# Kernel tuning notes

Measured on AMD Instinct MI355X. Metric: run time of the kernel, lower is better.

The kernel has to match this reference:

```python
import jax, jax.numpy as jnp
import numpy as np

ID, IH, IW = 8, 16, 16
HEADS, DIM_HEAD = 8, 32
INP, OUP = 256, 256
B = 4
N = ID * IH * IW  # 2048
INNER = HEADS * DIM_HEAD  # 256
SCALE = DIM_HEAD ** -0.5


def _make_relative_pos():
    # Faithful to the torch ctor: 3D coords, pairwise diffs, linearize, shift to >=0
    z, y, x = np.meshgrid(np.arange(ID), np.arange(IH), np.arange(IW), indexing='ij')
    coords = np.stack([z.ravel(), y.ravel(), x.ravel()], axis=1)  # [N,3]
    rel = coords[:, None, :] - coords[None, :, :]                 # [N,N,3]
    rp = rel[:, :, 0] * (IH * IW) + rel[:, :, 1] * IW + rel[:, :, 2]
    rp = rp - rp.min()
    return jnp.asarray(rp, dtype=jnp.int32)                       # [N,N]


def setup_inputs() -> dict:
    key = jax.random.key(0)
    k1, k2, k3, k4, k5 = jax.random.split(key, 5)
    table_size = ID * IH * IW * 8  # 16384, as in nn.Embedding ctor
    return {
        "x": jax.random.normal(k1, (B, N, INP), dtype=jnp.float32),
        "w_qkv": jax.random.normal(k2, (INP, 3 * INNER), dtype=jnp.float32) * (INP ** -0.5),
        "bias_table": jax.random.normal(k3, (table_size, 1), dtype=jnp.float32),
        "w_out": jax.random.normal(k4, (INNER, OUP), dtype=jnp.float32) * (INNER ** -0.5),
        "b_out": jax.random.normal(k5, (OUP,), dtype=jnp.float32),
        "relative_pos": _make_relative_pos(),
    }


def reference(x, w_qkv, bias_table, w_out, b_out, relative_pos):
    Bb, Nn, C = x.shape
    qkv = x @ w_qkv                                   # [B, N, 3*H*D]
    qkv = qkv.reshape(Bb, Nn, 3, HEADS, DIM_HEAD)
    qkv = jnp.transpose(qkv, (2, 0, 3, 1, 4))         # [3, B, H, N, D]
    q, k, v = qkv[0], qkv[1], qkv[2]
    q = q * SCALE
    attn = jnp.einsum('bhnd,bhmd->bhnm', q, k)        # [B, H, N, N]
    bias = bias_table[relative_pos, 0]                # [N, N], shared across B,H
    attn = attn + bias
    attn = jax.nn.softmax(attn, axis=-1)
    out = jnp.einsum('bhnm,bhmd->bhnd', attn, v)      # [B, H, N, D]
    out = jnp.transpose(out, (0, 2, 1, 3)).reshape(Bb, Nn, INNER)
    return out @ w_out + b_out                        # dropout p=0 -> identity
```

## Files before the change

kernel.cpp:

```cpp
#include <hip/hip_runtime.h>

typedef unsigned short u16;
typedef unsigned int u32;
typedef __attribute__((ext_vector_type(8))) short bf16x8;
typedef __attribute__((ext_vector_type(4))) short bf16x4;
typedef __attribute__((ext_vector_type(4))) float f32x4;

#define MFMA16(a, b, c) __builtin_amdgcn_mfma_f32_16x16x32_bf16(a, b, c, 0, 0, 0)
#define MFMAK16(a, b, c) __builtin_amdgcn_mfma_f32_16x16x16bf16_1k(a, b, c, 0, 0, 0)

__device__ __forceinline__ float hw_exp2(float x) { return __builtin_amdgcn_exp2f(x); }

__device__ __forceinline__ u16 f2bf(float f) {
    union { float f; u32 i; } v; v.f = f;
    u32 x = v.i;
    return (u16)((x + 0x7FFFu + ((x >> 16) & 1u)) >> 16);
}

__global__ __launch_bounds__(256) void k_prep(const float* __restrict__ x,
                                              const float* __restrict__ wqkv,
                                              const float* __restrict__ wout,
                                              u16* __restrict__ xb,
                                              u16* __restrict__ wqkvT,
                                              u16* __restrict__ woutT) {
    const float QSCALE2 = 0.2550566756538019f;
    int bx = blockIdx.x, tid = threadIdx.x;
    if (bx < 1024) {
        int base = bx * 2048 + tid * 8;
        float4 a = *(const float4*)(x + base);
        float4 b = *(const float4*)(x + base + 4);
        uint4 r;
        r.x = f2bf(a.x) | ((u32)f2bf(a.y) << 16);
        r.y = f2bf(a.z) | ((u32)f2bf(a.w) << 16);
        r.z = f2bf(b.x) | ((u32)f2bf(b.y) << 16);
        r.w = f2bf(b.z) | ((u32)f2bf(b.w) << 16);
        *(uint4*)(xb + base) = r;
    } else if (bx < 1792) {
        int idx = (bx - 1024) * 256 + tid;
        int n = idx >> 8, kk = idx & 255;
        float sc = (n < 256) ? QSCALE2 : 1.0f;
        wqkvT[idx] = f2bf(wqkv[kk * 768 + n] * sc);
    } else {
        int idx = (bx - 1792) * 256 + tid;
        int n = idx >> 8, kk = idx & 255;
        woutT[idx] = f2bf(wout[kk * 256 + n]);
    }
}

__global__ __launch_bounds__(256) void k_gemm_qkv(const u16* __restrict__ xb,
                                                  const u16* __restrict__ wT,
                                                  u16* __restrict__ qkv) {
    __shared__ __align__(16) u16 slds[8704];
    const int tid = threadIdx.x;
    const int wave = tid >> 6, lane = tid & 63, quad = lane >> 4, ql = lane & 15;
    const int mbase = blockIdx.x * 128 + (wave & 1) * 64;
    const int nbase = blockIdx.y * 64 + (wave >> 1) * 32;
    f32x4 acc[4][2];
#pragma unroll
    for (int i = 0; i < 4; ++i)
#pragma unroll
        for (int j = 0; j < 2; ++j) acc[i][j] = (f32x4){0.f, 0.f, 0.f, 0.f};
#pragma unroll
    for (int ks = 0; ks < 8; ++ks) {
        bf16x8 af[4], bfm[2];
#pragma unroll
        for (int ms = 0; ms < 4; ++ms)
            af[ms] = *(const bf16x8*)(xb + (size_t)(mbase + ms * 16 + ql) * 256 + ks * 32 + quad * 8);
#pragma unroll
        for (int ns = 0; ns < 2; ++ns)
            bfm[ns] = *(const bf16x8*)(wT + (size_t)(nbase + ns * 16 + ql) * 256 + ks * 32 + quad * 8);
#pragma unroll
        for (int ms = 0; ms < 4; ++ms)
#pragma unroll
            for (int ns = 0; ns < 2; ++ns)
                acc[ms][ns] = MFMA16(af[ms], bfm[ns], acc[ms][ns]);
    }

    const int t = (blockIdx.y * 64) >> 8;
    if (t < 2) {
        const int rowb = (wave & 1) * 64, colb = (wave >> 1) * 32;
#pragma unroll
        for (int ms = 0; ms < 4; ++ms)
#pragma unroll
            for (int ns = 0; ns < 2; ++ns)
#pragma unroll
                for (int r = 0; r < 4; ++r)
                    slds[(rowb + ms * 16 + quad * 4 + r) * 68 + colb + ns * 16 + ql] =
                        f2bf(acc[ms][ns][r]);
        __syncthreads();
        u16* base = qkv + (size_t)t * 2097152;
#pragma unroll
        for (int p = 0; p < 8; ++p) {
            int c = p * 256 + tid;
            int row = c >> 4, ch = c & 15;
            uint2 w = *(const uint2*)&slds[row * 68 + ch * 4];
            int n = blockIdx.x * 128 + row;
            int col = blockIdx.y * 64 + ch * 4;
            int h = (col & 255) >> 5, d = col & 31;
            *(uint2*)(base + ((size_t)((n >> 11) * 8 + h) * 2048 + (n & 2047)) * 32 + d) = w;
        }
    } else {
        const int hl = wave >> 1, nb = (wave & 1) * 64;
#pragma unroll
        for (int ms = 0; ms < 4; ++ms)
#pragma unroll
            for (int ns = 0; ns < 2; ++ns) {
                u16 e0 = f2bf(acc[ms][ns][0]), e1 = f2bf(acc[ms][ns][1]);
                u16 e2 = f2bf(acc[ms][ns][2]), e3 = f2bf(acc[ms][ns][3]);
                uint2 pp; pp.x = e0 | ((u32)e1 << 16); pp.y = e2 | ((u32)e3 << 16);
                *(uint2*)&slds[(hl * 32 + ns * 16 + ql) * 136 + nb + ms * 16 + quad * 4] = pp;
            }
        __syncthreads();
        u16* vbase = qkv + (size_t)2 * 2097152;
#pragma unroll
        for (int p = 0; p < 4; ++p) {
            int c = p * 256 + tid;
            int row = c >> 4, ch = c & 15;
            bf16x8 w = *(const bf16x8*)&slds[row * 136 + ch * 8];
            int n0 = blockIdx.x * 128 + ch * 8;
            int h = (blockIdx.y & 3) * 2 + (row >> 5), d = row & 31;
            *(bf16x8*)(vbase + (size_t)((n0 >> 11) * 8 + h) * 65536 +
                       (size_t)d * 2048 + (n0 & 2047)) = w;
        }
    }
}

__global__ __launch_bounds__(256, 2) void k_attn(const u16* __restrict__ q,
                                                 const u16* __restrict__ k,
                                                 const u16* __restrict__ vT,
                                                 const float* __restrict__ table,
                                                 u16* __restrict__ att) {
    __shared__ __align__(16) u16 kbuf[2][2][2048];
    __shared__ __align__(16) u16 vbuf[2][2][2048];
    __shared__ float tbl2[2176];
    const int tid = threadIdx.x;
    const int bh = blockIdx.x & 31, qt = blockIdx.x >> 5;
    const int wave = tid >> 6, lane = tid & 63, quad = lane >> 4, ql = lane & 15;
    const float LOG2E = 1.4426950408889634f;

    const u16* kbh = k + (size_t)bh * 65536;
    const u16* vbh = vT + (size_t)bh * 65536;

    const int krow = wave * 16 + (lane >> 2);
    const u16* kg = kbh + krow * 32 + ((((lane & 3) ^ ((lane >> 3) & 3))) << 3);
    const int vd = wave * 8 + (lane >> 3);
    const u16* vg = vbh + (size_t)vd * 2048 + (((lane & 7) ^ (vd & 7)) << 3);

#define GLDS(SRC, DST) __builtin_amdgcn_global_load_lds(                         \
        (const __attribute__((address_space(1))) void*)(SRC),                    \
        (__attribute__((address_space(3))) void*)(DST), 16, 0, 0)
#define DMA(BUF, PAIR) do {                                                      \
    GLDS(kg + (PAIR) * 4096,        &kbuf[BUF][0][wave * 512]);                  \
    GLDS(kg + (PAIR) * 4096 + 2048, &kbuf[BUF][1][wave * 512]);                  \
    GLDS(vg + (PAIR) * 128,         &vbuf[BUF][0][wave * 512]);                  \
    GLDS(vg + (PAIR) * 128 + 64,    &vbuf[BUF][1][wave * 512]);                  \
} while (0)

    DMA(0, 0);

    const float4* tg = (const float4*)(table + qt * 128);
    for (int i = tid; i < 544; i += 256) {
        float4 t = tg[i];
        t.x *= LOG2E; t.y *= LOG2E; t.z *= LOG2E; t.w *= LOG2E;
        ((float4*)tbl2)[i] = t;
    }

    const int qr0 = qt * 128 + wave * 32 + ql;
    bf16x8 qf[2];
    qf[0] = *(const bf16x8*)(q + ((size_t)bh * 2048 + qr0) * 32 + quad * 8);
    qf[1] = *(const bf16x8*)(q + ((size_t)bh * 2048 + qr0 + 16) * 32 + quad * 8);
    const int bloc0 = wave * 32 + ql + 2047 - quad * 4;
    const int kro = ((quad ^ ((ql >> 1) & 3)) << 3);

    bf16x4 ones4;
#pragma unroll
    for (int i = 0; i < 4; ++i) ones4[i] = (short)0x3F80;

    f32x4 oT0[2], oT1[2], oL[2];
#pragma unroll
    for (int qh = 0; qh < 2; ++qh) {
        oT0[qh] = (f32x4){0.f, 0.f, 0.f, 0.f};
        oT1[qh] = (f32x4){0.f, 0.f, 0.f, 0.f};
        oL[qh]  = (f32x4){0.f, 0.f, 0.f, 0.f};
    }

    __syncthreads();

    for (int pr = 0; pr < 16; ++pr) {
        const int buf = pr & 1;
        if (pr < 15) DMA(buf ^ 1, pr + 1);

#pragma unroll
        for (int t = 0; t < 2; ++t) {
            const int kt = pr * 2 + t;
            const u16* kb = &kbuf[buf][t][0];
            const u16* vb = &vbuf[buf][t][0];
            bf16x8 kf[4];
            bf16x4 va[2][4];
#pragma unroll
            for (int j = 0; j < 4; ++j)
                kf[j] = *(const bf16x8*)(kb + (j * 16 + ql) * 32 + kro);
#pragma unroll
            for (int dt = 0; dt < 2; ++dt)
#pragma unroll
                for (int j = 0; j < 4; ++j) {
                    int nloc = j * 16 + quad * 4;
                    int slot = (nloc >> 3) ^ (ql & 7);
                    va[dt][j] = *(const bf16x4*)(vb + (dt * 16 + ql) * 64 +
                                                 slot * 8 + (nloc & 7));
                }
            const int bkt = bloc0 - kt * 64;
            float bg[5][4];
#pragma unroll
            for (int g = 0; g < 5; ++g)
#pragma unroll
                for (int r = 0; r < 4; ++r)
                    bg[g][r] = tbl2[bkt + 16 * g - 48 - r];

#pragma unroll
            for (int qh = 0; qh < 2; ++qh) {
                f32x4 z = {0.f, 0.f, 0.f, 0.f};
                f32x4 s[4];
#pragma unroll
                for (int j = 0; j < 4; ++j) s[j] = MFMA16(kf[j], qf[qh], z);
#pragma unroll
                for (int j = 0; j < 4; ++j)
#pragma unroll
                    for (int r = 0; r < 4; ++r)
                        s[j][r] = hw_exp2(s[j][r] + bg[qh + 3 - j][r]);
#pragma unroll
                for (int j = 0; j < 4; ++j) {
                    union { u32 u[2]; bf16x4 v; } pj;
                    pj.u[0] = __builtin_amdgcn_perm(__float_as_uint(s[j][1]),
                                                    __float_as_uint(s[j][0]), 0x07060302u);
                    pj.u[1] = __builtin_amdgcn_perm(__float_as_uint(s[j][3]),
                                                    __float_as_uint(s[j][2]), 0x07060302u);
                    oT0[qh] = MFMAK16(va[0][j], pj.v, oT0[qh]);
                    oT1[qh] = MFMAK16(va[1][j], pj.v, oT1[qh]);
                    oL[qh]  = MFMAK16(ones4, pj.v, oL[qh]);
                }
            }
        }
        __syncthreads();
    }
#undef DMA
#undef GLDS

#pragma unroll
    for (int qh = 0; qh < 2; ++qh) {
        float inv = 1.0f / oL[qh][0];
        size_t base = ((size_t)bh * 2048 + qr0 + qh * 16) * 32;
#pragma unroll
        for (int dt = 0; dt < 2; ++dt) {
            const f32x4& o = dt ? oT1[qh] : oT0[qh];
            u16 e0 = f2bf(o[0] * inv), e1 = f2bf(o[1] * inv);
            u16 e2 = f2bf(o[2] * inv), e3 = f2bf(o[3] * inv);
            uint2 pp; pp.x = e0 | ((u32)e1 << 16); pp.y = e2 | ((u32)e3 << 16);
            *(uint2*)(att + base + dt * 16 + quad * 4) = pp;
        }
    }
}

__global__ __launch_bounds__(256) void k_gemm_out(const u16* __restrict__ attq,
                                                  const u16* __restrict__ wT,
                                                  const float* __restrict__ bout,
                                                  float* __restrict__ out) {
    const int tid = threadIdx.x;
    const int wave = tid >> 6, lane = tid & 63, quad = lane >> 4, ql = lane & 15;
    const int mbase = blockIdx.x * 128 + (wave & 1) * 64;
    const int nbase = blockIdx.y * 64 + (wave >> 1) * 32;
    f32x4 acc[4][2];
#pragma unroll
    for (int i = 0; i < 4; ++i)
#pragma unroll
        for (int j = 0; j < 2; ++j) acc[i][j] = (f32x4){0.f, 0.f, 0.f, 0.f};
#pragma unroll
    for (int ks = 0; ks < 8; ++ks) {
        bf16x8 af[4], bfm[2];
#pragma unroll
        for (int ms = 0; ms < 4; ++ms) {
            int row = mbase + ms * 16 + ql;
            af[ms] = *(const bf16x8*)(attq +
                ((size_t)((row >> 11) * 8 + ks) * 2048 + (row & 2047)) * 32 + quad * 8);
        }
#pragma unroll
        for (int ns = 0; ns < 2; ++ns)
            bfm[ns] = *(const bf16x8*)(wT + (size_t)(nbase + ns * 16 + ql) * 256 + ks * 32 + quad * 8);
#pragma unroll
        for (int ms = 0; ms < 4; ++ms)
#pragma unroll
            for (int ns = 0; ns < 2; ++ns)
                acc[ms][ns] = MFMA16(af[ms], bfm[ns], acc[ms][ns]);
    }
#pragma unroll
    for (int ms = 0; ms < 4; ++ms)
#pragma unroll
        for (int ns = 0; ns < 2; ++ns)
#pragma unroll
            for (int r = 0; r < 4; ++r) {
                int Mrow = mbase + ms * 16 + quad * 4 + r;
                int col = nbase + ns * 16 + ql;
                out[(size_t)Mrow * 256 + col] = acc[ms][ns][r] + bout[col];
            }
}

extern "C" void kernel_launch(void* const* d_in, const int* in_sizes, int n_in,
                              void* d_out, int out_size, void* d_ws, size_t ws_size,
                              hipStream_t stream) {
    const float* x    = (const float*)d_in[0];
    const float* wqkv = (const float*)d_in[1];
    const float* btab = (const float*)d_in[2];
    const float* wout = (const float*)d_in[3];
    const float* bout = (const float*)d_in[4];
    float* out = (float*)d_out;

    if (ws_size < (size_t)13107200) return;
    u16* ws = (u16*)d_ws;
    u16* wqkvT = ws;
    u16* woutT = wqkvT + 196608;
    u16* qkv   = woutT + 65536;
    u16* xb    = (u16*)d_out;

    hipLaunchKernelGGL(k_prep, dim3(2048), dim3(256), 0, stream, x, wqkv, wout, xb, wqkvT, woutT);
    hipLaunchKernelGGL(k_gemm_qkv, dim3(64, 12), dim3(256), 0, stream, xb, wqkvT, qkv);
    hipLaunchKernelGGL(k_attn, dim3(512), dim3(256), 0, stream,
                       qkv, qkv + 2097152, qkv + 2 * 2097152, btab, qkv);
    hipLaunchKernelGGL(k_gemm_out, dim3(64, 4), dim3(256), 0, stream, qkv, woutT, bout, out);
}
```

Measured before the change: 142.0 us.

## Fold relative-position bias into MFMA accumulator and read it from global

Pre-scales the bias table by log2(e) once in the prep kernel into a workspace buffer. The attention kernel drops its LDS bias table and instead loads bias values straight from global (L1/L2-cached) at the start of each key-tile pair, before the DMA issue. The bias becomes the MFMA accumulator input, which removes the separate add before exp2. This cuts LDS use and one VALU add per score, at the cost of extra global loads per iteration and more registers held live for the bias values.

```diff
diff --git a/kernel.cpp b/kernel.cpp
--- a/kernel.cpp
+++ b/kernel.cpp
@@ -20,10 +20,13 @@
 __global__ __launch_bounds__(256) void k_prep(const float* __restrict__ x,
                                               const float* __restrict__ wqkv,
                                               const float* __restrict__ wout,
+                                              const float* __restrict__ btab,
                                               u16* __restrict__ xb,
                                               u16* __restrict__ wqkvT,
-                                              u16* __restrict__ woutT) {
+                                              u16* __restrict__ woutT,
+                                              float* __restrict__ stab) {
     const float QSCALE2 = 0.2550566756538019f;
+    const float LOG2E = 1.4426950408889634f;
     int bx = blockIdx.x, tid = threadIdx.x;
     if (bx < 1024) {
         int base = bx * 2048 + tid * 8;
@@ -40,10 +43,13 @@
         int n = idx >> 8, kk = idx & 255;
         float sc = (n < 256) ? QSCALE2 : 1.0f;
         wqkvT[idx] = f2bf(wqkv[kk * 768 + n] * sc);
-    } else {
+    } else if (bx < 2048) {
         int idx = (bx - 1792) * 256 + tid;
         int n = idx >> 8, kk = idx & 255;
         woutT[idx] = f2bf(wout[kk * 256 + n]);
+    } else {
+        int idx = (bx - 2048) * 256 + tid;
+        stab[idx] = btab[idx] * LOG2E;
     }
 }
 
@@ -128,15 +134,13 @@
 __global__ __launch_bounds__(256, 2) void k_attn(const u16* __restrict__ q,
                                                  const u16* __restrict__ k,
                                                  const u16* __restrict__ vT,
-                                                 const float* __restrict__ table,
+                                                 const float* __restrict__ stab,
                                                  u16* __restrict__ att) {
     __shared__ __align__(16) u16 kbuf[2][2][2048];
     __shared__ __align__(16) u16 vbuf[2][2][2048];
-    __shared__ float tbl2[2176];
     const int tid = threadIdx.x;
     const int bh = blockIdx.x & 31, qt = blockIdx.x >> 5;
     const int wave = tid >> 6, lane = tid & 63, quad = lane >> 4, ql = lane & 15;
-    const float LOG2E = 1.4426950408889634f;
 
     const u16* kbh = k + (size_t)bh * 65536;
     const u16* vbh = vT + (size_t)bh * 65536;
@@ -158,12 +162,7 @@
 
     DMA(0, 0);
 
-    const float4* tg = (const float4*)(table + qt * 128);
-    for (int i = tid; i < 544; i += 256) {
-        float4 t = tg[i];
-        t.x *= LOG2E; t.y *= LOG2E; t.z *= LOG2E; t.w *= LOG2E;
-        ((float4*)tbl2)[i] = t;
-    }
+    const float* gtab = stab + qt * 128;
 
     const int qr0 = qt * 128 + wave * 32 + ql;
     bf16x8 qf[2];
@@ -188,11 +187,23 @@
 
     for (int pr = 0; pr < 16; ++pr) {
         const int buf = pr & 1;
+
+        f32x4 bc[2][5];
+#pragma unroll
+        for (int t = 0; t < 2; ++t) {
+            const int bkt = bloc0 - (pr * 2 + t) * 64;
+#pragma unroll
+            for (int g = 0; g < 5; ++g) {
+                const float* p = gtab + (bkt + 16 * g - 51);
+                bc[t][g] = (f32x4){p[3], p[2], p[1], p[0]};
+            }
+        }
+        __builtin_amdgcn_sched_barrier(0);
+
         if (pr < 15) DMA(buf ^ 1, pr + 1);
 
 #pragma unroll
         for (int t = 0; t < 2; ++t) {
-            const int kt = pr * 2 + t;
             const u16* kb = &kbuf[buf][t][0];
             const u16* vb = &vbuf[buf][t][0];
             bf16x8 kf[4];
@@ -209,25 +220,18 @@
                     va[dt][j] = *(const bf16x4*)(vb + (dt * 16 + ql) * 64 +
                                                  slot * 8 + (nloc & 7));
                 }
-            const int bkt = bloc0 - kt * 64;
-            float bg[5][4];
-#pragma unroll
-            for (int g = 0; g < 5; ++g)
-#pragma unroll
-                for (int r = 0; r < 4; ++r)
-                    bg[g][r] = tbl2[bkt + 16 * g - 48 - r];
 
 #pragma unroll
             for (int qh = 0; qh < 2; ++qh) {
-                f32x4 z = {0.f, 0.f, 0.f, 0.f};
                 f32x4 s[4];
 #pragma unroll
-                for (int j = 0; j < 4; ++j) s[j] = MFMA16(kf[j], qf[qh], z);
-#pragma unroll
                 for (int j = 0; j < 4; ++j)
+                    s[j] = MFMA16(kf[j], qf[qh], bc[t][qh + 3 - j]);
+#pragma unroll
+                for (int j = 0; j < 4; ++j)
 #pragma unroll
                     for (int r = 0; r < 4; ++r)
-                        s[j][r] = hw_exp2(s[j][r] + bg[qh + 3 - j][r]);
+                        s[j][r] = hw_exp2(s[j][r]);
 #pragma unroll
                 for (int j = 0; j < 4; ++j) {
                     union { u32 u[2]; bf16x4 v; } pj;
@@ -314,16 +318,18 @@
     const float* bout = (const float*)d_in[4];
     float* out = (float*)d_out;
 
-    if (ws_size < (size_t)13107200) return;
+    if (ws_size < (size_t)13172736) return;
     u16* ws = (u16*)d_ws;
     u16* wqkvT = ws;
     u16* woutT = wqkvT + 196608;
     u16* qkv   = woutT + 65536;
+    float* stab = (float*)(qkv + 6291456);
     u16* xb    = (u16*)d_out;
 
-    hipLaunchKernelGGL(k_prep, dim3(2048), dim3(256), 0, stream, x, wqkv, wout, xb, wqkvT, woutT);
+    hipLaunchKernelGGL(k_prep, dim3(2112), dim3(256), 0, stream, x, wqkv, wout, btab,
+                       xb, wqkvT, woutT, stab);
     hipLaunchKernelGGL(k_gemm_qkv, dim3(64, 12), dim3(256), 0, stream, xb, wqkvT, qkv);
     hipLaunchKernelGGL(k_attn, dim3(512), dim3(256), 0, stream,
-                       qkv, qkv + 2097152, qkv + 2 * 2097152, btab, qkv);
+                       qkv, qkv + 2097152, qkv + 2 * 2097152, stab, qkv);
     hipLaunchKernelGGL(k_gemm_out, dim3(64, 4), dim3(256), 0, stream, qkv, woutT, bout, out);
 }
```

Result: no change. 141.1 us (-0.7%).

## Fuse fp32-to-bf16 conversion into GEMMs and fold bias into MFMA accumulator

Applied to the files above, without the earlier changes.

Drops the separate prep kernel. The QKV GEMM now reads fp32 x directly and packs it to bf16 in registers. Both GEMMs transpose and convert their weight slice into LDS at block start. In attention, the relative-position bias is preloaded per pair of key tiles and passed as the MFMA accumulator init, removing the separate add before exp2. This saves one launch and the xb/weight round trip through memory, but each block re-converts weights and reads twice as many bytes of x.

```diff
diff --git a/kernel.cpp b/kernel.cpp
--- a/kernel.cpp
+++ b/kernel.cpp
@@ -17,44 +17,39 @@
     return (u16)((x + 0x7FFFu + ((x >> 16) & 1u)) >> 16);
 }
 
-__global__ __launch_bounds__(256) void k_prep(const float* __restrict__ x,
-                                              const float* __restrict__ wqkv,
-                                              const float* __restrict__ wout,
-                                              u16* __restrict__ xb,
-                                              u16* __restrict__ wqkvT,
-                                              u16* __restrict__ woutT) {
-    const float QSCALE2 = 0.2550566756538019f;
-    int bx = blockIdx.x, tid = threadIdx.x;
-    if (bx < 1024) {
-        int base = bx * 2048 + tid * 8;
-        float4 a = *(const float4*)(x + base);
-        float4 b = *(const float4*)(x + base + 4);
-        uint4 r;
-        r.x = f2bf(a.x) | ((u32)f2bf(a.y) << 16);
-        r.y = f2bf(a.z) | ((u32)f2bf(a.w) << 16);
-        r.z = f2bf(b.x) | ((u32)f2bf(b.y) << 16);
-        r.w = f2bf(b.z) | ((u32)f2bf(b.w) << 16);
-        *(uint4*)(xb + base) = r;
-    } else if (bx < 1792) {
-        int idx = (bx - 1024) * 256 + tid;
-        int n = idx >> 8, kk = idx & 255;
-        float sc = (n < 256) ? QSCALE2 : 1.0f;
-        wqkvT[idx] = f2bf(wqkv[kk * 768 + n] * sc);
-    } else {
-        int idx = (bx - 1792) * 256 + tid;
-        int n = idx >> 8, kk = idx & 255;
-        woutT[idx] = f2bf(wout[kk * 256 + n]);
-    }
-}
-
-__global__ __launch_bounds__(256) void k_gemm_qkv(const u16* __restrict__ xb,
-                                                  const u16* __restrict__ wT,
+__device__ __forceinline__ bf16x8 pack8(float4 a, float4 b) {
+    bf16x8 r;
+    r[0] = (short)f2bf(a.x); r[1] = (short)f2bf(a.y);
+    r[2] = (short)f2bf(a.z); r[3] = (short)f2bf(a.w);
+    r[4] = (short)f2bf(b.x); r[5] = (short)f2bf(b.y);
+    r[6] = (short)f2bf(b.z); r[7] = (short)f2bf(b.w);
+    return r;
+}
+
+__global__ __launch_bounds__(256) void k_gemm_qkv(const float* __restrict__ x,
+                                                  const float* __restrict__ wqkv,
                                                   u16* __restrict__ qkv) {
-    __shared__ __align__(16) u16 slds[8704];
+    __shared__ __align__(16) u16 smem[16896];
     const int tid = threadIdx.x;
     const int wave = tid >> 6, lane = tid & 63, quad = lane >> 4, ql = lane & 15;
+    const int by = blockIdx.y;
     const int mbase = blockIdx.x * 128 + (wave & 1) * 64;
-    const int nbase = blockIdx.y * 64 + (wave >> 1) * 32;
+    const float QSCALE2 = 0.2550566756538019f;
+
+    {
+        const int c4 = (tid & 15) * 4;
+        const float sc = (by < 4) ? QSCALE2 : 1.0f;
+        for (int kk = tid >> 4; kk < 256; kk += 16) {
+            float4 w4 = *(const float4*)(wqkv + (size_t)kk * 768 + by * 64 + c4);
+            smem[(c4 + 0) * 264 + kk] = f2bf(w4.x * sc);
+            smem[(c4 + 1) * 264 + kk] = f2bf(w4.y * sc);
+            smem[(c4 + 2) * 264 + kk] = f2bf(w4.z * sc);
+            smem[(c4 + 3) * 264 + kk] = f2bf(w4.w * sc);
+        }
+    }
+    __syncthreads();
+
+    const int nrow = (wave >> 1) * 32;
     f32x4 acc[4][2];
 #pragma unroll
     for (int i = 0; i < 4; ++i)
@@ -64,19 +59,23 @@
     for (int ks = 0; ks < 8; ++ks) {
         bf16x8 af[4], bfm[2];
 #pragma unroll
-        for (int ms = 0; ms < 4; ++ms)
-            af[ms] = *(const bf16x8*)(xb + (size_t)(mbase + ms * 16 + ql) * 256 + ks * 32 + quad * 8);
+        for (int ms = 0; ms < 4; ++ms) {
+            const float* ap = x + (size_t)(mbase + ms * 16 + ql) * 256 + ks * 32 + quad * 8;
+            af[ms] = pack8(*(const float4*)ap, *(const float4*)(ap + 4));
+        }
 #pragma unroll
         for (int ns = 0; ns < 2; ++ns)
-            bfm[ns] = *(const bf16x8*)(wT + (size_t)(nbase + ns * 16 + ql) * 256 + ks * 32 + quad * 8);
+            bfm[ns] = *(const bf16x8*)&smem[(nrow + ns * 16 + ql) * 264 + ks * 32 + quad * 8];
 #pragma unroll
         for (int ms = 0; ms < 4; ++ms)
 #pragma unroll
             for (int ns = 0; ns < 2; ++ns)
                 acc[ms][ns] = MFMA16(af[ms], bfm[ns], acc[ms][ns]);
     }
-
-    const int t = (blockIdx.y * 64) >> 8;
+    __syncthreads();
+
+    u16* slds = smem;
+    const int t = (by * 64) >> 8;
     if (t < 2) {
         const int rowb = (wave & 1) * 64, colb = (wave >> 1) * 32;
 #pragma unroll
@@ -95,7 +94,7 @@
             int row = c >> 4, ch = c & 15;
             uint2 w = *(const uint2*)&slds[row * 68 + ch * 4];
             int n = blockIdx.x * 128 + row;
-            int col = blockIdx.y * 64 + ch * 4;
+            int col = by * 64 + ch * 4;
             int h = (col & 255) >> 5, d = col & 31;
             *(uint2*)(base + ((size_t)((n >> 11) * 8 + h) * 2048 + (n & 2047)) * 32 + d) = w;
         }
@@ -118,7 +117,7 @@
             int row = c >> 4, ch = c & 15;
             bf16x8 w = *(const bf16x8*)&slds[row * 136 + ch * 8];
             int n0 = blockIdx.x * 128 + ch * 8;
-            int h = (blockIdx.y & 3) * 2 + (row >> 5), d = row & 31;
+            int h = (by & 3) * 2 + (row >> 5), d = row & 31;
             *(bf16x8*)(vbase + (size_t)((n0 >> 11) * 8 + h) * 65536 +
                        (size_t)d * 2048 + (n0 & 2047)) = w;
         }
@@ -188,11 +187,23 @@
 
     for (int pr = 0; pr < 16; ++pr) {
         const int buf = pr & 1;
+
+        f32x4 bc[2][5];
+#pragma unroll
+        for (int t = 0; t < 2; ++t) {
+            const int bkt = bloc0 - (pr * 2 + t) * 64;
+#pragma unroll
+            for (int g = 0; g < 5; ++g) {
+                const int b0 = bkt + 16 * g - 51;
+                bc[t][g] = (f32x4){tbl2[b0 + 3], tbl2[b0 + 2], tbl2[b0 + 1], tbl2[b0 + 0]};
+            }
+        }
+        __builtin_amdgcn_sched_barrier(0);
+
         if (pr < 15) DMA(buf ^ 1, pr + 1);
 
 #pragma unroll
         for (int t = 0; t < 2; ++t) {
-            const int kt = pr * 2 + t;
             const u16* kb = &kbuf[buf][t][0];
             const u16* vb = &vbuf[buf][t][0];
             bf16x8 kf[4];
@@ -209,25 +220,18 @@
                     va[dt][j] = *(const bf16x4*)(vb + (dt * 16 + ql) * 64 +
                                                  slot * 8 + (nloc & 7));
                 }
-            const int bkt = bloc0 - kt * 64;
-            float bg[5][4];
-#pragma unroll
-            for (int g = 0; g < 5; ++g)
-#pragma unroll
-                for (int r = 0; r < 4; ++r)
-                    bg[g][r] = tbl2[bkt + 16 * g - 48 - r];
 
 #pragma unroll
             for (int qh = 0; qh < 2; ++qh) {
-                f32x4 z = {0.f, 0.f, 0.f, 0.f};
                 f32x4 s[4];
 #pragma unroll
-                for (int j = 0; j < 4; ++j) s[j] = MFMA16(kf[j], qf[qh], z);
-#pragma unroll
                 for (int j = 0; j < 4; ++j)
+                    s[j] = MFMA16(kf[j], qf[qh], bc[t][qh + 3 - j]);
+#pragma unroll
+                for (int j = 0; j < 4; ++j)
 #pragma unroll
                     for (int r = 0; r < 4; ++r)
-                        s[j][r] = hw_exp2(s[j][r] + bg[qh + 3 - j][r]);
+                        s[j][r] = hw_exp2(s[j][r]);
 #pragma unroll
                 for (int j = 0; j < 4; ++j) {
                     union { u32 u[2]; bf16x4 v; } pj;
@@ -262,13 +266,28 @@
 }
 
 __global__ __launch_bounds__(256) void k_gemm_out(const u16* __restrict__ attq,
-                                                  const u16* __restrict__ wT,
+                                                  const float* __restrict__ wout,
                                                   const float* __restrict__ bout,
                                                   float* __restrict__ out) {
+    __shared__ __align__(16) u16 bs[16896];
     const int tid = threadIdx.x;
     const int wave = tid >> 6, lane = tid & 63, quad = lane >> 4, ql = lane & 15;
+    const int by = blockIdx.y;
     const int mbase = blockIdx.x * 128 + (wave & 1) * 64;
-    const int nbase = blockIdx.y * 64 + (wave >> 1) * 32;
+
+    {
+        const int c4 = (tid & 15) * 4;
+        for (int kk = tid >> 4; kk < 256; kk += 16) {
+            float4 w4 = *(const float4*)(wout + (size_t)kk * 256 + by * 64 + c4);
+            bs[(c4 + 0) * 264 + kk] = f2bf(w4.x);
+            bs[(c4 + 1) * 264 + kk] = f2bf(w4.y);
+            bs[(c4 + 2) * 264 + kk] = f2bf(w4.z);
+            bs[(c4 + 3) * 264 + kk] = f2bf(w4.w);
+        }
+    }
+    __syncthreads();
+
+    const int nrow = (wave >> 1) * 32;
     f32x4 acc[4][2];
 #pragma unroll
     for (int i = 0; i < 4; ++i)
@@ -285,7 +304,7 @@
         }
 #pragma unroll
         for (int ns = 0; ns < 2; ++ns)
-            bfm[ns] = *(const bf16x8*)(wT + (size_t)(nbase + ns * 16 + ql) * 256 + ks * 32 + quad * 8);
+            bfm[ns] = *(const bf16x8*)&bs[(nrow + ns * 16 + ql) * 264 + ks * 32 + quad * 8];
 #pragma unroll
         for (int ms = 0; ms < 4; ++ms)
 #pragma unroll
@@ -299,7 +318,7 @@
 #pragma unroll
             for (int r = 0; r < 4; ++r) {
                 int Mrow = mbase + ms * 16 + quad * 4 + r;
-                int col = nbase + ns * 16 + ql;
+                int col = by * 64 + (wave >> 1) * 32 + ns * 16 + ql;
                 out[(size_t)Mrow * 256 + col] = acc[ms][ns][r] + bout[col];
             }
 }
@@ -314,16 +333,11 @@
     const float* bout = (const float*)d_in[4];
     float* out = (float*)d_out;
 
-    if (ws_size < (size_t)13107200) return;
-    u16* ws = (u16*)d_ws;
-    u16* wqkvT = ws;
-    u16* woutT = wqkvT + 196608;
-    u16* qkv   = woutT + 65536;
-    u16* xb    = (u16*)d_out;
-
-    hipLaunchKernelGGL(k_prep, dim3(2048), dim3(256), 0, stream, x, wqkv, wout, xb, wqkvT, woutT);
-    hipLaunchKernelGGL(k_gemm_qkv, dim3(64, 12), dim3(256), 0, stream, xb, wqkvT, qkv);
+    if (ws_size < (size_t)12582912) return;
+    u16* qkv = (u16*)d_ws;
+
+    hipLaunchKernelGGL(k_gemm_qkv, dim3(64, 12), dim3(256), 0, stream, x, wqkv, qkv);
     hipLaunchKernelGGL(k_attn, dim3(512), dim3(256), 0, stream,
                        qkv, qkv + 2097152, qkv + 2 * 2097152, btab, qkv);
-    hipLaunchKernelGGL(k_gemm_out, dim3(64, 4), dim3(256), 0, stream, qkv, woutT, bout, out);
-}
+    hipLaunchKernelGGL(k_gemm_out, dim3(64, 4), dim3(256), 0, stream, qkv, wout, bout, out);
+}
```

Result: no change. 143.5 us (+1.1%).
